# Kernel optimization log

Measured on AMD Instinct MI355X. Metric: run time of the kernel, lower is better.

Reference implementation:

```python
import jax, jax.numpy as jnp
import numpy as np

N_USERS = 500_000
N_ITEMS = 200_000
D_FEAT = 256
H = 32
N_EDGES = 2_000_000
NEG_SLOPE = 0.01


def _lin(k, out_dim, in_dim):
    return jax.random.normal(k, (out_dim, in_dim), jnp.float32) * (1.0 / np.sqrt(in_dim))


def setup_inputs() -> dict:
    key = jax.random.key(0)
    ks = jax.random.split(key, 24)
    src = jax.random.randint(ks[0], (N_EDGES,), 0, N_USERS)   # user ids
    dst = jax.random.randint(ks[1], (N_EDGES,), 0, N_ITEMS)   # product ids
    inp = {
        "user_ids": jnp.arange(N_USERS, dtype=jnp.int32),
        "product_ids": jnp.arange(N_ITEMS, dtype=jnp.int32),
        "product_features": jax.random.normal(ks[2], (N_ITEMS, D_FEAT), jnp.float32),
        "edge_rates": jnp.stack([src, dst]),      # user -> product
        "edge_rated_by": jnp.stack([dst, src]),   # product -> user (reverse)
        "user_emb": jax.random.normal(ks[3], (N_USERS, H), jnp.float32),
        "item_emb": jax.random.normal(ks[4], (N_ITEMS, H), jnp.float32),
        "feat_W": _lin(ks[5], H, D_FEAT),
        "feat_b": jnp.zeros((H,), jnp.float32),
    }
    # SAGEConv params: lin_l (neighbor, with bias), lin_r (root, no bias)
    names = ["up1", "pu1", "up2", "pu2"]  # up = user->product conv, pu = product->user conv
    for i, n in enumerate(names):
        inp[f"Wl_{n}"] = _lin(ks[6 + 3 * i], H, H)
        inp[f"bl_{n}"] = jnp.zeros((H,), jnp.float32)
        inp[f"Wr_{n}"] = _lin(ks[7 + 3 * i], H, H)
    return inp


def _sage(x_src, x_dst, edge_index, Wl, bl, Wr):
    # PyG SAGEConv, aggr='mean': lin_l(mean_j x_src[j]) + lin_r(x_dst)
    e_src, e_dst = edge_index[0], edge_index[1]
    n_dst = x_dst.shape[0]
    msg_sum = jax.ops.segment_sum(x_src[e_src], e_dst, num_segments=n_dst)
    cnt = jax.ops.segment_sum(jnp.ones_like(e_dst, dtype=x_src.dtype), e_dst, num_segments=n_dst)
    mean = msg_sum / jnp.maximum(cnt, 1.0)[:, None]
    return mean @ Wl.T + bl + x_dst @ Wr.T


def reference(user_ids, product_ids, product_features, edge_rates, edge_rated_by,
              user_emb, item_emb, feat_W, feat_b,
              Wl_up1, bl_up1, Wr_up1, Wl_pu1, bl_pu1, Wr_pu1,
              Wl_up2, bl_up2, Wr_up2, Wl_pu2, bl_pu2, Wr_pu2):
    lrelu = lambda x: jax.nn.leaky_relu(x, NEG_SLOPE)
    xu = user_emb[user_ids]                                    # [Nu, H]
    xp = item_emb[product_ids] + product_features @ feat_W.T + feat_b  # [Ni, H]

    # layer 1 (HeteroConv: each node type has exactly one incoming relation)
    p1 = lrelu(_sage(xu, xp, edge_rates, Wl_up1, bl_up1, Wr_up1))
    u1 = lrelu(_sage(xp, xu, edge_rated_by, Wl_pu1, bl_pu1, Wr_pu1))
    # layer 2
    p2 = lrelu(_sage(u1, p1, edge_rates, Wl_up2, bl_up2, Wr_up2))
    u2 = lrelu(_sage(p1, u1, edge_rated_by, Wl_pu2, bl_pu2, Wr_pu2))

    final_user = jnp.concatenate([xu, u1, u2], axis=1)   # [Nu, 3H]
    final_item = jnp.concatenate([xp, p1, p2], axis=1)   # [Ni, 3H]
    return final_user, final_item
```

## Files before the change

kernel.cpp:

```cpp
#include <hip/hip_runtime.h>

#define NU 500000
#define NI 200000
#define NN (NU + NI)
#define NE 2000000
#define HD 32
#define DF 256
#define OC 96

typedef float        f4 __attribute__((ext_vector_type(4)));
typedef unsigned int u2 __attribute__((ext_vector_type(2)));
typedef unsigned int u4v __attribute__((ext_vector_type(4)));
typedef unsigned short ushort_t;

__device__ __forceinline__ float lrelu(float v){ return v >= 0.f ? v : 0.01f*v; }

__device__ __forceinline__ unsigned int f2bf(float f){
  unsigned int u = __float_as_uint(f);
  u += 0x7fffu + ((u >> 16) & 1u);
  return u >> 16;
}
__device__ __forceinline__ float bflo(unsigned int u){ return __uint_as_float(u << 16); }
__device__ __forceinline__ float bfhi(unsigned int u){ return __uint_as_float(u & 0xffff0000u); }

__global__ void k_zero_i32(int* __restrict__ p, int n){
  int i = blockIdx.x*blockDim.x + threadIdx.x;
  if (i < n) p[i] = 0;
}

__global__ void k_init_user(const int* __restrict__ ids, const float* __restrict__ emb,
                            float* __restrict__ outu){
  int i = blockIdx.x*blockDim.x + threadIdx.x;
  if (i >= NU) return;
  int uid = ids[i];
  const f4* s = (const f4*)(emb + (size_t)uid*HD);
  f4* d = (f4*)(outu + (size_t)i*OC);
  #pragma unroll
  for (int q = 0; q < 8; ++q) {
    f4 v = __builtin_nontemporal_load(s + q);
    __builtin_nontemporal_store(v, d + q);
  }
}

__global__ __launch_bounds__(512) void k_init_item(
    const int* __restrict__ ids, const float* __restrict__ emb,
    const float* __restrict__ feat, const float* __restrict__ W,
    const float* __restrict__ bias, float* __restrict__ outi){
  __shared__ float combo[256*34];
  int t = threadIdx.x;
  int r = t & 255;
  int seg = __builtin_amdgcn_readfirstlane(t >> 8);
  int row = blockIdx.x*256 + r;
  bool valid = row < NI;
  float acc[HD];
  #pragma unroll
  for (int h = 0; h < HD; ++h) acc[h] = 0.f;

  if (valid) {
    const f4* f4p = (const f4*)(feat + (size_t)row*DF + seg*128);
    f4 a0 = __builtin_nontemporal_load(f4p);
    f4 a1 = __builtin_nontemporal_load(f4p + 1);
    for (int k0 = 0; k0 < 128; k0 += 8) {
      f4 n0 = {0,0,0,0}, n1 = {0,0,0,0};
      if (k0 + 8 < 128) {
        n0 = __builtin_nontemporal_load(f4p + (k0>>2) + 2);
        n1 = __builtin_nontemporal_load(f4p + (k0>>2) + 3);
      }
      float fv[8] = {a0.x,a0.y,a0.z,a0.w,a1.x,a1.y,a1.z,a1.w};
      #pragma unroll
      for (int kk = 0; kk < 8; ++kk) {
        #pragma unroll
        for (int h = 0; h < HD; ++h)
          acc[h] += fv[kk]*W[h*DF + seg*128 + k0 + kk];
      }
      a0 = n0; a1 = n1;
    }
  }
  if (seg == 1) {
    float2* c2 = (float2*)(combo + r*34);
    #pragma unroll
    for (int q = 0; q < 16; ++q) c2[q] = make_float2(acc[2*q], acc[2*q+1]);
  }
  __syncthreads();
  if (seg == 0 && valid) {
    const float2* c2 = (const float2*)(combo + r*34);
    #pragma unroll
    for (int q = 0; q < 16; ++q) { float2 v = c2[q]; acc[2*q] += v.x; acc[2*q+1] += v.y; }
    int pid = ids[row];
    const f4* ev = (const f4*)(emb + (size_t)pid*HD);
    const f4* bv = (const f4*)bias;
    f4* dst = (f4*)(outi + (size_t)row*OC);
    #pragma unroll
    for (int q = 0; q < 8; ++q) {
      f4 e = ev[q], b = bv[q];
      f4 o;
      o.x = acc[4*q+0]+e.x+b.x; o.y = acc[4*q+1]+e.y+b.y;
      o.z = acc[4*q+2]+e.z+b.z; o.w = acc[4*q+3]+e.w+b.w;
      __builtin_nontemporal_store(o, dst + q);
    }
  }
}

__global__ void k_deg(const int* __restrict__ esrc, const int* __restrict__ edst,
                      int* __restrict__ cnt){
  int e = blockIdx.x*blockDim.x + threadIdx.x;
  if (e >= NE) return;
  int u = __builtin_nontemporal_load(esrc + e);
  int p = __builtin_nontemporal_load(edst + e);
  atomicAdd(cnt + u, 1);
  atomicAdd(cnt + NU + p, 1);
}

__global__ void k_scan1(const int* __restrict__ cnt, int* __restrict__ off,
                        int* __restrict__ part, int n){
  __shared__ int s[256];
  int t = threadIdx.x, i = blockIdx.x*256 + t;
  int v = (i < n) ? cnt[i] : 0;
  s[t] = v; __syncthreads();
  for (int o = 1; o < 256; o <<= 1) {
    int x = (t >= o) ? s[t-o] : 0;
    __syncthreads(); s[t] += x; __syncthreads();
  }
  if (i < n) off[i] = s[t] - v;
  if (t == 255) part[blockIdx.x] = s[255];
}

__global__ void k_scan2(int* __restrict__ part, int nb){
  __shared__ int s[256];
  __shared__ int carry;
  int t = threadIdx.x;
  if (t == 0) carry = 0;
  __syncthreads();
  for (int c0 = 0; c0 < nb; c0 += 256) {
    int i = c0 + t;
    int v = (i < nb) ? part[i] : 0;
    s[t] = v; __syncthreads();
    for (int o = 1; o < 256; o <<= 1) {
      int x = (t >= o) ? s[t-o] : 0;
      __syncthreads(); s[t] += x; __syncthreads();
    }
    int total = s[255];
    if (i < nb) part[i] = carry + s[t] - v;
    __syncthreads();
    if (t == 0) carry += total;
    __syncthreads();
  }
}

__global__ void k_scan3(int* __restrict__ off, const int* __restrict__ part, int n){
  int i = blockIdx.x*256 + threadIdx.x;
  if (i < n) off[i] += part[blockIdx.x];
}

__global__ void k_scatter(const int* __restrict__ esrc, const int* __restrict__ edst,
                          const int* __restrict__ off, int* __restrict__ cur,
                          int* __restrict__ partner){
  int e = blockIdx.x*blockDim.x + threadIdx.x;
  if (e >= NE) return;
  int u = __builtin_nontemporal_load(esrc + e);
  int p = __builtin_nontemporal_load(edst + e);
  int s1 = off[u]      + atomicAdd(cur + u,      1);
  int s2 = off[NU + p] + atomicAdd(cur + NU + p, 1);
  partner[s1] = s2;
  partner[s2] = s1;
}

__global__ void k_mat(const float* __restrict__ srcbase, int scol, int n_src, int nodebase,
                      const int* __restrict__ off, const int* __restrict__ cnt,
                      const int* __restrict__ partner, ushort_t* __restrict__ edgeval,
                      int slotbase){
  int tid = blockIdx.x*256 + threadIdx.x;
  int node = tid >> 3;
  if (node >= n_src) return;
  int q = tid & 7;
  int gnode = nodebase + node;
  int deg = cnt[gnode];
  if (deg <= 0) return;
  int start = off[gnode];
  f4 v = __builtin_nontemporal_load((const f4*)(srcbase + (size_t)node*OC + scol) + q);
  u2 pv; pv.x = f2bf(v.x) | (f2bf(v.y) << 16); pv.y = f2bf(v.z) | (f2bf(v.w) << 16);
  u2* ev = (u2*)edgeval + q;
  int j = 0;
  for (; j + 4 <= deg; j += 4) {
    int s0 = __builtin_nontemporal_load(partner + start + j + 0) - slotbase;
    int s1 = __builtin_nontemporal_load(partner + start + j + 1) - slotbase;
    int s2 = __builtin_nontemporal_load(partner + start + j + 2) - slotbase;
    int s3 = __builtin_nontemporal_load(partner + start + j + 3) - slotbase;
    __builtin_nontemporal_store(pv, ev + (size_t)s0*8);
    __builtin_nontemporal_store(pv, ev + (size_t)s1*8);
    __builtin_nontemporal_store(pv, ev + (size_t)s2*8);
    __builtin_nontemporal_store(pv, ev + (size_t)s3*8);
  }
  for (; j < deg; ++j) {
    int s = __builtin_nontemporal_load(partner + start + j) - slotbase;
    __builtin_nontemporal_store(pv, ev + (size_t)s*8);
  }
}

__global__ void k_aggsum(const ushort_t* __restrict__ edgeval, int slotbase,
                         int n, int nodebase,
                         const int* __restrict__ off, const int* __restrict__ cnt,
                         ushort_t* __restrict__ meanb){
  int tid = blockIdx.x*256 + threadIdx.x;
  int node = tid >> 3;
  if (node >= n) return;
  int q = tid & 7;
  int gnode = nodebase + node;
  int deg = cnt[gnode];
  int start = off[gnode] - slotbase;
  const u2* ev = (const u2*)edgeval + q;
  f4 a0 = {0,0,0,0}, a1 = a0, a2 = a0, a3 = a0;
  int j = 0;
  for (; j + 4 <= deg; j += 4) {
    u2 r0 = ev[(size_t)(start+j+0)*8];
    u2 r1 = ev[(size_t)(start+j+1)*8];
    u2 r2 = ev[(size_t)(start+j+2)*8];
    u2 r3 = ev[(size_t)(start+j+3)*8];
    a0.x += bflo(r0.x); a0.y += bfhi(r0.x); a0.z += bflo(r0.y); a0.w += bfhi(r0.y);
    a1.x += bflo(r1.x); a1.y += bfhi(r1.x); a1.z += bflo(r1.y); a1.w += bfhi(r1.y);
    a2.x += bflo(r2.x); a2.y += bfhi(r2.x); a2.z += bflo(r2.y); a2.w += bfhi(r2.y);
    a3.x += bflo(r3.x); a3.y += bfhi(r3.x); a3.z += bflo(r3.y); a3.w += bfhi(r3.y);
  }
  for (; j < deg; ++j) {
    u2 r = ev[(size_t)(start+j)*8];
    a0.x += bflo(r.x); a0.y += bfhi(r.x); a0.z += bflo(r.y); a0.w += bfhi(r.y);
  }
  a0 += a1 + a2 + a3;
  float inv = (deg > 0) ? 1.f/(float)deg : 0.f;
  u2 pv;
  pv.x = f2bf(a0.x*inv) | (f2bf(a0.y*inv) << 16);
  pv.y = f2bf(a0.z*inv) | (f2bf(a0.w*inv) << 16);
  *((u2*)meanb + (size_t)node*8 + q) = pv;
}

__global__ void k_fin2(float* __restrict__ dstbase, int n,
                       const ushort_t* __restrict__ meanb, int xoff, int outoff,
                       const float* __restrict__ Wl, const float* __restrict__ bl,
                       const float* __restrict__ Wr){
  int i = blockIdx.x*blockDim.x + threadIdx.x;
  if (i >= n) return;
  float m[HD], x[HD];
  const u4v* mb = (const u4v*)(meanb + (size_t)i*HD);
  #pragma unroll
  for (int t = 0; t < 4; ++t) {
    u4v v = mb[t];
    m[8*t+0] = bflo(v.x); m[8*t+1] = bfhi(v.x);
    m[8*t+2] = bflo(v.y); m[8*t+3] = bfhi(v.y);
    m[8*t+4] = bflo(v.z); m[8*t+5] = bfhi(v.z);
    m[8*t+6] = bflo(v.w); m[8*t+7] = bfhi(v.w);
  }
  float* row = dstbase + (size_t)i*OC;
  #pragma unroll
  for (int qq = 0; qq < 8; ++qq) {
    f4 xx = *((const f4*)(row + xoff) + qq);
    x[4*qq+0]=xx.x; x[4*qq+1]=xx.y; x[4*qq+2]=xx.z; x[4*qq+3]=xx.w;
  }
  float y[HD];
  #pragma unroll
  for (int h = 0; h < HD; ++h) {
    float s = bl[h];
    #pragma unroll
    for (int j = 0; j < HD; ++j) s += m[j]*Wl[h*HD+j];
    #pragma unroll
    for (int j = 0; j < HD; ++j) s += x[j]*Wr[h*HD+j];
    y[h] = lrelu(s);
  }
  #pragma unroll
  for (int qq = 0; qq < 8; ++qq) {
    f4 yo; yo.x=y[4*qq+0]; yo.y=y[4*qq+1]; yo.z=y[4*qq+2]; yo.w=y[4*qq+3];
    __builtin_nontemporal_store(yo, (f4*)(row + outoff) + qq);
  }
}

__global__ void k_aggfin(float* __restrict__ dstbase, int n, int nodebase,
                         const ushort_t* __restrict__ edgeval, int slotbase,
                         int xoff, int outoff,
                         const int* __restrict__ off, const int* __restrict__ cnt,
                         const float* __restrict__ Wl, const float* __restrict__ bl,
                         const float* __restrict__ Wr){
  int tid = blockIdx.x*256 + threadIdx.x;
  int node = tid >> 3;
  if (node >= n) return;
  int q = tid & 7;
  int gnode = nodebase + node;
  int deg = cnt[gnode];
  int start = off[gnode] - slotbase;
  f4 xv = *((const f4*)(dstbase + (size_t)node*OC + xoff) + q);
  const u2* ev = (const u2*)edgeval + q;
  f4 a0 = {0,0,0,0};
  for (int j = 0; j < deg; ++j) {
    u2 r = ev[(size_t)(start+j)*8];
    a0.x += bflo(r.x); a0.y += bfhi(r.x); a0.z += bflo(r.y); a0.w += bfhi(r.y);
  }
  float inv = (deg > 0) ? 1.f/(float)deg : 0.f;
  float m0[4] = {a0.x*inv, a0.y*inv, a0.z*inv, a0.w*inv};
  float x0[4] = {xv.x, xv.y, xv.z, xv.w};
  bool b1 = (q & 1), b2 = (q & 2), b4 = (q & 4);
  float tm1[8], tx1[8];
  #pragma unroll
  for (int k = 0; k < 4; ++k) {
    float om = __shfl_xor(m0[k], 1), ox = __shfl_xor(x0[k], 1);
    tm1[k]   = b1 ? om    : m0[k];  tx1[k]   = b1 ? ox    : x0[k];
    tm1[k+4] = b1 ? m0[k] : om;     tx1[k+4] = b1 ? x0[k] : ox;
  }
  float tm2[16], tx2[16];
  #pragma unroll
  for (int k = 0; k < 8; ++k) {
    float om = __shfl_xor(tm1[k], 2), ox = __shfl_xor(tx1[k], 2);
    tm2[k]   = b2 ? om     : tm1[k];  tx2[k]   = b2 ? ox     : tx1[k];
    tm2[k+8] = b2 ? tm1[k] : om;      tx2[k+8] = b2 ? tx1[k] : ox;
  }
  float m[32], x[32];
  #pragma unroll
  for (int k = 0; k < 16; ++k) {
    float om = __shfl_xor(tm2[k], 4), ox = __shfl_xor(tx2[k], 4);
    m[k]    = b4 ? om     : tm2[k];  x[k]    = b4 ? ox     : tx2[k];
    m[k+16] = b4 ? tm2[k] : om;      x[k+16] = b4 ? tx2[k] : ox;
  }
  float y[4];
  #pragma unroll
  for (int k = 0; k < 4; ++k) {
    int h = q*4 + k;
    float s = bl[h];
    const f4* wl = (const f4*)(Wl + h*HD);
    const f4* wr = (const f4*)(Wr + h*HD);
    #pragma unroll
    for (int j4 = 0; j4 < 8; ++j4) {
      f4 wv = wl[j4];
      s += m[4*j4+0]*wv.x + m[4*j4+1]*wv.y + m[4*j4+2]*wv.z + m[4*j4+3]*wv.w;
    }
    #pragma unroll
    for (int j4 = 0; j4 < 8; ++j4) {
      f4 wv = wr[j4];
      s += x[4*j4+0]*wv.x + x[4*j4+1]*wv.y + x[4*j4+2]*wv.z + x[4*j4+3]*wv.w;
    }
    y[k] = lrelu(s);
  }
  f4 yo; yo.x = y[0]; yo.y = y[1]; yo.z = y[2]; yo.w = y[3];
  *((f4*)(dstbase + (size_t)node*OC + outoff) + q) = yo;
}

extern "C" void kernel_launch(void* const* d_in, const int* in_sizes, int n_in,
                              void* d_out, int out_size, void* d_ws, size_t ws_size,
                              hipStream_t stream) {
  const int*   user_ids = (const int*)d_in[0];
  const int*   prod_ids = (const int*)d_in[1];
  const float* feat     = (const float*)d_in[2];
  const int*   er       = (const int*)d_in[3];
  const float* uemb     = (const float*)d_in[5];
  const float* iemb     = (const float*)d_in[6];
  const float* fW       = (const float*)d_in[7];
  const float* fb       = (const float*)d_in[8];
  const float* Wl_up1 = (const float*)d_in[9];
  const float* bl_up1 = (const float*)d_in[10];
  const float* Wr_up1 = (const float*)d_in[11];
  const float* Wl_pu1 = (const float*)d_in[12];
  const float* bl_pu1 = (const float*)d_in[13];
  const float* Wr_pu1 = (const float*)d_in[14];
  const float* Wl_up2 = (const float*)d_in[15];
  const float* bl_up2 = (const float*)d_in[16];
  const float* Wr_up2 = (const float*)d_in[17];
  const float* Wl_pu2 = (const float*)d_in[18];
  const float* bl_pu2 = (const float*)d_in[19];
  const float* Wr_pu2 = (const float*)d_in[20];

  float* outu = (float*)d_out;
  float* outi = outu + (size_t)NU*OC;

  int* cnt  = (int*)d_ws;
  int* cur  = cnt + NN;
  int* off  = cur + NN;
  int* part = off + NN;
  int* pn   = part + 2736;
  size_t base_bytes = ((size_t)3*NN + 2736 + 2*(size_t)NE) * 4;
  size_t ev_off = (base_bytes + 255) & ~(size_t)255;
  ushort_t* edgeval = (ushort_t*)((char*)d_ws + ev_off);
  size_t mb_off = ev_off + (size_t)NE*64;
  ushort_t* meanb = (ushort_t*)((char*)d_ws + mb_off);
  bool have_mean = ws_size >= mb_off + (size_t)NU*64;

  const int* er_src = er;
  const int* er_dst = er + NE;

  const int B = 256;
  const int NB1 = (NN + 255)/256;
  const int GU8 = ((size_t)NU*8 + B - 1)/B, GI8 = ((size_t)NI*8 + B - 1)/B;
  const int GU1 = (NU + B - 1)/B,           GI1 = (NI + B - 1)/B;

  k_zero_i32<<<(2*NN + B - 1)/B, B, 0, stream>>>(cnt, 2*NN);
  k_deg<<<(NE + B - 1)/B, B, 0, stream>>>(er_src, er_dst, cnt);
  k_scan1<<<NB1, B, 0, stream>>>(cnt, off, part, NN);
  k_scan2<<<1, B, 0, stream>>>(part, NB1);
  k_scan3<<<NB1, B, 0, stream>>>(off, part, NN);
  k_scatter<<<(NE + B - 1)/B, B, 0, stream>>>(er_src, er_dst, off, cur, pn);

  k_init_user<<<GU1, B, 0, stream>>>(user_ids, uemb, outu);
  k_init_item<<<(NI + 255)/256, 512, 0, stream>>>(prod_ids, iemb, feat, fW, fb, outi);

  if (have_mean) {
    k_mat<<<GU8, B, 0, stream>>>(outu, 0, NU, 0, off, cnt, pn, edgeval, NE);
    k_aggsum<<<GI8, B, 0, stream>>>(edgeval, NE, NI, NU, off, cnt, meanb);
    k_fin2<<<GI1, B, 0, stream>>>(outi, NI, meanb, 0, 32, Wl_up1, bl_up1, Wr_up1);
    k_mat<<<GI8, B, 0, stream>>>(outi, 0, NI, NU, off, cnt, pn, edgeval, 0);
    k_aggsum<<<GU8, B, 0, stream>>>(edgeval, 0, NU, 0, off, cnt, meanb);
    k_fin2<<<GU1, B, 0, stream>>>(outu, NU, meanb, 0, 32, Wl_pu1, bl_pu1, Wr_pu1);
    k_mat<<<GU8, B, 0, stream>>>(outu, 32, NU, 0, off, cnt, pn, edgeval, NE);
    k_aggsum<<<GI8, B, 0, stream>>>(edgeval, NE, NI, NU, off, cnt, meanb);
    k_fin2<<<GI1, B, 0, stream>>>(outi, NI, meanb, 32, 64, Wl_up2, bl_up2, Wr_up2);
    k_mat<<<GI8, B, 0, stream>>>(outi, 32, NI, NU, off, cnt, pn, edgeval, 0);
    k_aggsum<<<GU8, B, 0, stream>>>(edgeval, 0, NU, 0, off, cnt, meanb);
    k_fin2<<<GU1, B, 0, stream>>>(outu, NU, meanb, 32, 64, Wl_pu2, bl_pu2, Wr_pu2);
  } else {
    k_mat<<<GU8, B, 0, stream>>>(outu, 0, NU, 0, off, cnt, pn, edgeval, NE);
    k_aggfin<<<GI8, B, 0, stream>>>(outi, NI, NU, edgeval, NE, 0, 32, off, cnt,
                                    Wl_up1, bl_up1, Wr_up1);
    k_mat<<<GI8, B, 0, stream>>>(outi, 0, NI, NU, off, cnt, pn, edgeval, 0);
    k_aggfin<<<GU8, B, 0, stream>>>(outu, NU, 0, edgeval, 0, 0, 32, off, cnt,
                                    Wl_pu1, bl_pu1, Wr_pu1);
    k_mat<<<GU8, B, 0, stream>>>(outu, 32, NU, 0, off, cnt, pn, edgeval, NE);
    k_aggfin<<<GI8, B, 0, stream>>>(outi, NI, NU, edgeval, NE, 32, 64, off, cnt,
                                    Wl_up2, bl_up2, Wr_up2);
    k_mat<<<GI8, B, 0, stream>>>(outi, 32, NI, NU, off, cnt, pn, edgeval, 0);
    k_aggfin<<<GU8, B, 0, stream>>>(outu, NU, 0, edgeval, 0, 32, 64, off, cnt,
                                    Wl_pu2, bl_pu2, Wr_pu2);
  }
}
```

Baseline: 1.764 ms.

## Fuse init with edge materialization, use MFMA for item features, merge aggregate+finalize

The user-embedding copy is fused with the first edge-value scatter, so the user table is written once and also packed into a compact bf16 table. The item feature projection now runs on bf16 MFMA tiles instead of scalar FMA. The separate aggregate, mean-buffer and finalize kernels are replaced by one kernel that stages per-node means in shared memory and also writes a bf16 copy of the layer-1 user output. The next scatter reads that compact table instead of the fp32 rows, and nontemporal hints are dropped. This cuts kernel launches and intermediate traffic, at the cost of bf16 rounding in the feature GEMM and a workspace size assumption that is no longer checked.

```diff
diff --git a/kernel.cpp b/kernel.cpp
--- a/kernel.cpp
+++ b/kernel.cpp
@@ -8,9 +8,9 @@
 #define DF 256
 #define OC 96
 
-typedef float        f4 __attribute__((ext_vector_type(4)));
-typedef unsigned int u2 __attribute__((ext_vector_type(2)));
-typedef unsigned int u4v __attribute__((ext_vector_type(4)));
+typedef float        f4  __attribute__((ext_vector_type(4)));
+typedef unsigned int u2  __attribute__((ext_vector_type(2)));
+typedef short        s8v __attribute__((ext_vector_type(8)));
 typedef unsigned short ushort_t;
 
 __device__ __forceinline__ float lrelu(float v){ return v >= 0.f ? v : 0.01f*v; }
@@ -23,82 +23,16 @@
 __device__ __forceinline__ float bflo(unsigned int u){ return __uint_as_float(u << 16); }
 __device__ __forceinline__ float bfhi(unsigned int u){ return __uint_as_float(u & 0xffff0000u); }
 
+__device__ __forceinline__ s8v pack8(f4 a, f4 b){
+  s8v r;
+  r[0]=(short)f2bf(a.x); r[1]=(short)f2bf(a.y); r[2]=(short)f2bf(a.z); r[3]=(short)f2bf(a.w);
+  r[4]=(short)f2bf(b.x); r[5]=(short)f2bf(b.y); r[6]=(short)f2bf(b.z); r[7]=(short)f2bf(b.w);
+  return r;
+}
+
 __global__ void k_zero_i32(int* __restrict__ p, int n){
   int i = blockIdx.x*blockDim.x + threadIdx.x;
   if (i < n) p[i] = 0;
-}
-
-__global__ void k_init_user(const int* __restrict__ ids, const float* __restrict__ emb,
-                            float* __restrict__ outu){
-  int i = blockIdx.x*blockDim.x + threadIdx.x;
-  if (i >= NU) return;
-  int uid = ids[i];
-  const f4* s = (const f4*)(emb + (size_t)uid*HD);
-  f4* d = (f4*)(outu + (size_t)i*OC);
-  #pragma unroll
-  for (int q = 0; q < 8; ++q) {
-    f4 v = __builtin_nontemporal_load(s + q);
-    __builtin_nontemporal_store(v, d + q);
-  }
-}
-
-__global__ __launch_bounds__(512) void k_init_item(
-    const int* __restrict__ ids, const float* __restrict__ emb,
-    const float* __restrict__ feat, const float* __restrict__ W,
-    const float* __restrict__ bias, float* __restrict__ outi){
-  __shared__ float combo[256*34];
-  int t = threadIdx.x;
-  int r = t & 255;
-  int seg = __builtin_amdgcn_readfirstlane(t >> 8);
-  int row = blockIdx.x*256 + r;
-  bool valid = row < NI;
-  float acc[HD];
-  #pragma unroll
-  for (int h = 0; h < HD; ++h) acc[h] = 0.f;
-
-  if (valid) {
-    const f4* f4p = (const f4*)(feat + (size_t)row*DF + seg*128);
-    f4 a0 = __builtin_nontemporal_load(f4p);
-    f4 a1 = __builtin_nontemporal_load(f4p + 1);
-    for (int k0 = 0; k0 < 128; k0 += 8) {
-      f4 n0 = {0,0,0,0}, n1 = {0,0,0,0};
-      if (k0 + 8 < 128) {
-        n0 = __builtin_nontemporal_load(f4p + (k0>>2) + 2);
-        n1 = __builtin_nontemporal_load(f4p + (k0>>2) + 3);
-      }
-      float fv[8] = {a0.x,a0.y,a0.z,a0.w,a1.x,a1.y,a1.z,a1.w};
-      #pragma unroll
-      for (int kk = 0; kk < 8; ++kk) {
-        #pragma unroll
-        for (int h = 0; h < HD; ++h)
-          acc[h] += fv[kk]*W[h*DF + seg*128 + k0 + kk];
-      }
-      a0 = n0; a1 = n1;
-    }
-  }
-  if (seg == 1) {
-    float2* c2 = (float2*)(combo + r*34);
-    #pragma unroll
-    for (int q = 0; q < 16; ++q) c2[q] = make_float2(acc[2*q], acc[2*q+1]);
-  }
-  __syncthreads();
-  if (seg == 0 && valid) {
-    const float2* c2 = (const float2*)(combo + r*34);
-    #pragma unroll
-    for (int q = 0; q < 16; ++q) { float2 v = c2[q]; acc[2*q] += v.x; acc[2*q+1] += v.y; }
-    int pid = ids[row];
-    const f4* ev = (const f4*)(emb + (size_t)pid*HD);
-    const f4* bv = (const f4*)bias;
-    f4* dst = (f4*)(outi + (size_t)row*OC);
-    #pragma unroll
-    for (int q = 0; q < 8; ++q) {
-      f4 e = ev[q], b = bv[q];
-      f4 o;
-      o.x = acc[4*q+0]+e.x+b.x; o.y = acc[4*q+1]+e.y+b.y;
-      o.z = acc[4*q+2]+e.z+b.z; o.w = acc[4*q+3]+e.w+b.w;
-      __builtin_nontemporal_store(o, dst + q);
-    }
-  }
 }
 
 __global__ void k_deg(const int* __restrict__ esrc, const int* __restrict__ edst,
@@ -165,10 +99,88 @@
   partner[s2] = s1;
 }
 
-__global__ void k_mat(const float* __restrict__ srcbase, int scol, int n_src, int nodebase,
-                      const int* __restrict__ off, const int* __restrict__ cnt,
-                      const int* __restrict__ partner, ushort_t* __restrict__ edgeval,
-                      int slotbase){
+__global__ void k_init_user_mat(const int* __restrict__ ids, const float* __restrict__ emb,
+                                float* __restrict__ outu, ushort_t* __restrict__ tbl,
+                                const int* __restrict__ off, const int* __restrict__ cnt,
+                                const int* __restrict__ partner,
+                                ushort_t* __restrict__ edgeval){
+  int tid = blockIdx.x*256 + threadIdx.x;
+  int node = tid >> 3;
+  if (node >= NU) return;
+  int q = tid & 7;
+  int uid = ids[node];
+  f4 v = *((const f4*)(emb + (size_t)uid*HD) + q);
+  *((f4*)(outu + (size_t)node*OC) + q) = v;
+  u2 pv; pv.x = f2bf(v.x) | (f2bf(v.y) << 16); pv.y = f2bf(v.z) | (f2bf(v.w) << 16);
+  ((u2*)tbl)[(size_t)node*8 + q] = pv;
+  int deg = cnt[node];
+  if (deg <= 0) return;
+  int start = off[node];
+  u2* ev = (u2*)edgeval + q;
+  int j = 0;
+  for (; j + 4 <= deg; j += 4) {
+    int s0 = __builtin_nontemporal_load(partner + start + j + 0) - NE;
+    int s1 = __builtin_nontemporal_load(partner + start + j + 1) - NE;
+    int s2 = __builtin_nontemporal_load(partner + start + j + 2) - NE;
+    int s3 = __builtin_nontemporal_load(partner + start + j + 3) - NE;
+    ev[(size_t)s0*8] = pv; ev[(size_t)s1*8] = pv;
+    ev[(size_t)s2*8] = pv; ev[(size_t)s3*8] = pv;
+  }
+  for (; j < deg; ++j) {
+    int s = __builtin_nontemporal_load(partner + start + j) - NE;
+    ev[(size_t)s*8] = pv;
+  }
+}
+
+__global__ __launch_bounds__(256) void k_init_item_mfma(
+    const int* __restrict__ ids, const float* __restrict__ emb,
+    const float* __restrict__ feat, const float* __restrict__ W,
+    const float* __restrict__ bias, float* __restrict__ outi){
+  int wave = threadIdx.x >> 6;
+  int lane = threadIdx.x & 63;
+  int tile = blockIdx.x*4 + wave;
+  int row0 = tile*16;
+  if (row0 >= NI) return;
+  int m = lane & 15, grp = lane >> 4;
+
+  s8v bfrag[16];
+  #pragma unroll
+  for (int ks = 0; ks < 8; ++ks) {
+    #pragma unroll
+    for (int nh = 0; nh < 2; ++nh) {
+      const float* wp = W + (size_t)(nh*16 + m)*DF + ks*32 + grp*8;
+      f4 w0 = *(const f4*)wp;
+      f4 w1 = *(const f4*)(wp + 4);
+      bfrag[ks*2 + nh] = pack8(w0, w1);
+    }
+  }
+
+  f4 acc0 = {0,0,0,0}, acc1 = {0,0,0,0};
+  const float* fr = feat + (size_t)(row0 + m)*DF + grp*8;
+  #pragma unroll
+  for (int ks = 0; ks < 8; ++ks) {
+    f4 a0 = *(const f4*)(fr + ks*32);
+    f4 a1 = *(const f4*)(fr + ks*32 + 4);
+    s8v af = pack8(a0, a1);
+    acc0 = __builtin_amdgcn_mfma_f32_16x16x32_bf16(af, bfrag[ks*2+0], acc0, 0, 0, 0);
+    acc1 = __builtin_amdgcn_mfma_f32_16x16x32_bf16(af, bfrag[ks*2+1], acc1, 0, 0, 0);
+  }
+
+  #pragma unroll
+  for (int j = 0; j < 4; ++j) {
+    int r = row0 + grp*4 + j;
+    int pid = ids[r];
+    float v0 = acc0[j] + emb[(size_t)pid*HD + m]      + bias[m];
+    float v1 = acc1[j] + emb[(size_t)pid*HD + 16 + m] + bias[16 + m];
+    outi[(size_t)r*OC + m]      = v0;
+    outi[(size_t)r*OC + 16 + m] = v1;
+  }
+}
+
+__global__ void k_mat_f32(const float* __restrict__ srcbase, int scol, int n_src, int nodebase,
+                          const int* __restrict__ off, const int* __restrict__ cnt,
+                          const int* __restrict__ partner, ushort_t* __restrict__ edgeval,
+                          int slotbase){
   int tid = blockIdx.x*256 + threadIdx.x;
   int node = tid >> 3;
   if (node >= n_src) return;
@@ -177,7 +189,7 @@
   int deg = cnt[gnode];
   if (deg <= 0) return;
   int start = off[gnode];
-  f4 v = __builtin_nontemporal_load((const f4*)(srcbase + (size_t)node*OC + scol) + q);
+  f4 v = *((const f4*)(srcbase + (size_t)node*OC + scol) + q);
   u2 pv; pv.x = f2bf(v.x) | (f2bf(v.y) << 16); pv.y = f2bf(v.z) | (f2bf(v.w) << 16);
   u2* ev = (u2*)edgeval + q;
   int j = 0;
@@ -186,137 +198,91 @@
     int s1 = __builtin_nontemporal_load(partner + start + j + 1) - slotbase;
     int s2 = __builtin_nontemporal_load(partner + start + j + 2) - slotbase;
     int s3 = __builtin_nontemporal_load(partner + start + j + 3) - slotbase;
-    __builtin_nontemporal_store(pv, ev + (size_t)s0*8);
-    __builtin_nontemporal_store(pv, ev + (size_t)s1*8);
-    __builtin_nontemporal_store(pv, ev + (size_t)s2*8);
-    __builtin_nontemporal_store(pv, ev + (size_t)s3*8);
+    ev[(size_t)s0*8] = pv; ev[(size_t)s1*8] = pv;
+    ev[(size_t)s2*8] = pv; ev[(size_t)s3*8] = pv;
   }
   for (; j < deg; ++j) {
     int s = __builtin_nontemporal_load(partner + start + j) - slotbase;
-    __builtin_nontemporal_store(pv, ev + (size_t)s*8);
-  }
-}
-
-__global__ void k_aggsum(const ushort_t* __restrict__ edgeval, int slotbase,
-                         int n, int nodebase,
-                         const int* __restrict__ off, const int* __restrict__ cnt,
-                         ushort_t* __restrict__ meanb){
+    ev[(size_t)s*8] = pv;
+  }
+}
+
+__global__ void k_mat_tbl(const ushort_t* __restrict__ tbl, int n_src, int nodebase,
+                          const int* __restrict__ off, const int* __restrict__ cnt,
+                          const int* __restrict__ partner, ushort_t* __restrict__ edgeval,
+                          int slotbase){
   int tid = blockIdx.x*256 + threadIdx.x;
   int node = tid >> 3;
-  if (node >= n) return;
+  if (node >= n_src) return;
   int q = tid & 7;
   int gnode = nodebase + node;
   int deg = cnt[gnode];
-  int start = off[gnode] - slotbase;
-  const u2* ev = (const u2*)edgeval + q;
-  f4 a0 = {0,0,0,0}, a1 = a0, a2 = a0, a3 = a0;
+  if (deg <= 0) return;
+  int start = off[gnode];
+  u2 pv = ((const u2*)tbl)[(size_t)node*8 + q];
+  u2* ev = (u2*)edgeval + q;
   int j = 0;
   for (; j + 4 <= deg; j += 4) {
-    u2 r0 = ev[(size_t)(start+j+0)*8];
-    u2 r1 = ev[(size_t)(start+j+1)*8];
-    u2 r2 = ev[(size_t)(start+j+2)*8];
-    u2 r3 = ev[(size_t)(start+j+3)*8];
-    a0.x += bflo(r0.x); a0.y += bfhi(r0.x); a0.z += bflo(r0.y); a0.w += bfhi(r0.y);
-    a1.x += bflo(r1.x); a1.y += bfhi(r1.x); a1.z += bflo(r1.y); a1.w += bfhi(r1.y);
-    a2.x += bflo(r2.x); a2.y += bfhi(r2.x); a2.z += bflo(r2.y); a2.w += bfhi(r2.y);
-    a3.x += bflo(r3.x); a3.y += bfhi(r3.x); a3.z += bflo(r3.y); a3.w += bfhi(r3.y);
+    int s0 = __builtin_nontemporal_load(partner + start + j + 0) - slotbase;
+    int s1 = __builtin_nontemporal_load(partner + start + j + 1) - slotbase;
+    int s2 = __builtin_nontemporal_load(partner + start + j + 2) - slotbase;
+    int s3 = __builtin_nontemporal_load(partner + start + j + 3) - slotbase;
+    ev[(size_t)s0*8] = pv; ev[(size_t)s1*8] = pv;
+    ev[(size_t)s2*8] = pv; ev[(size_t)s3*8] = pv;
   }
   for (; j < deg; ++j) {
-    u2 r = ev[(size_t)(start+j)*8];
-    a0.x += bflo(r.x); a0.y += bfhi(r.x); a0.z += bflo(r.y); a0.w += bfhi(r.y);
-  }
-  a0 += a1 + a2 + a3;
+    int s = __builtin_nontemporal_load(partner + start + j) - slotbase;
+    ev[(size_t)s*8] = pv;
+  }
+}
+
+__global__ __launch_bounds__(256) void k_aggfin2(
+    float* __restrict__ dstbase, int n, int nodebase,
+    const ushort_t* __restrict__ edgeval, int slotbase,
+    int xoff, int outoff,
+    const int* __restrict__ off, const int* __restrict__ cnt,
+    const float* __restrict__ Wl, const float* __restrict__ bl,
+    const float* __restrict__ Wr, ushort_t* __restrict__ tblout){
+  __shared__ float mbuf[32*36];
+  __shared__ float xbuf[32*36];
+  int t = threadIdx.x;
+  int nl = t >> 3;
+  int q = t & 7;
+  int node = blockIdx.x*32 + nl;
+  bool valid = node < n;
+  f4 a0 = {0,0,0,0}, a1 = a0, a2 = a0, a3 = a0, xv = a0;
+  int deg = 0;
+  if (valid) {
+    int g = nodebase + node;
+    deg = cnt[g];
+    int start = off[g] - slotbase;
+    xv = *((const f4*)(dstbase + (size_t)node*OC + xoff) + q);
+    const u2* ev = (const u2*)edgeval + q;
+    int j = 0;
+    for (; j + 4 <= deg; j += 4) {
+      u2 r0 = ev[(size_t)(start+j+0)*8];
+      u2 r1 = ev[(size_t)(start+j+1)*8];
+      u2 r2 = ev[(size_t)(start+j+2)*8];
+      u2 r3 = ev[(size_t)(start+j+3)*8];
+      a0.x += bflo(r0.x); a0.y += bfhi(r0.x); a0.z += bflo(r0.y); a0.w += bfhi(r0.y);
+      a1.x += bflo(r1.x); a1.y += bfhi(r1.x); a1.z += bflo(r1.y); a1.w += bfhi(r1.y);
+      a2.x += bflo(r2.x); a2.y += bfhi(r2.x); a2.z += bflo(r2.y); a2.w += bfhi(r2.y);
+      a3.x += bflo(r3.x); a3.y += bfhi(r3.x); a3.z += bflo(r3.y); a3.w += bfhi(r3.y);
+    }
+    for (; j < deg; ++j) {
+      u2 r = ev[(size_t)(start+j)*8];
+      a0.x += bflo(r.x); a0.y += bfhi(r.x); a0.z += bflo(r.y); a0.w += bfhi(r.y);
+    }
+    a0 += a1 + a2 + a3;
+  }
   float inv = (deg > 0) ? 1.f/(float)deg : 0.f;
-  u2 pv;
-  pv.x = f2bf(a0.x*inv) | (f2bf(a0.y*inv) << 16);
-  pv.y = f2bf(a0.z*inv) | (f2bf(a0.w*inv) << 16);
-  *((u2*)meanb + (size_t)node*8 + q) = pv;
-}
-
-__global__ void k_fin2(float* __restrict__ dstbase, int n,
-                       const ushort_t* __restrict__ meanb, int xoff, int outoff,
-                       const float* __restrict__ Wl, const float* __restrict__ bl,
-                       const float* __restrict__ Wr){
-  int i = blockIdx.x*blockDim.x + threadIdx.x;
-  if (i >= n) return;
-  float m[HD], x[HD];
-  const u4v* mb = (const u4v*)(meanb + (size_t)i*HD);
-  #pragma unroll
-  for (int t = 0; t < 4; ++t) {
-    u4v v = mb[t];
-    m[8*t+0] = bflo(v.x); m[8*t+1] = bfhi(v.x);
-    m[8*t+2] = bflo(v.y); m[8*t+3] = bfhi(v.y);
-    m[8*t+4] = bflo(v.z); m[8*t+5] = bfhi(v.z);
-    m[8*t+6] = bflo(v.w); m[8*t+7] = bfhi(v.w);
-  }
-  float* row = dstbase + (size_t)i*OC;
-  #pragma unroll
-  for (int qq = 0; qq < 8; ++qq) {
-    f4 xx = *((const f4*)(row + xoff) + qq);
-    x[4*qq+0]=xx.x; x[4*qq+1]=xx.y; x[4*qq+2]=xx.z; x[4*qq+3]=xx.w;
-  }
-  float y[HD];
-  #pragma unroll
-  for (int h = 0; h < HD; ++h) {
-    float s = bl[h];
-    #pragma unroll
-    for (int j = 0; j < HD; ++j) s += m[j]*Wl[h*HD+j];
-    #pragma unroll
-    for (int j = 0; j < HD; ++j) s += x[j]*Wr[h*HD+j];
-    y[h] = lrelu(s);
-  }
-  #pragma unroll
-  for (int qq = 0; qq < 8; ++qq) {
-    f4 yo; yo.x=y[4*qq+0]; yo.y=y[4*qq+1]; yo.z=y[4*qq+2]; yo.w=y[4*qq+3];
-    __builtin_nontemporal_store(yo, (f4*)(row + outoff) + qq);
-  }
-}
-
-__global__ void k_aggfin(float* __restrict__ dstbase, int n, int nodebase,
-                         const ushort_t* __restrict__ edgeval, int slotbase,
-                         int xoff, int outoff,
-                         const int* __restrict__ off, const int* __restrict__ cnt,
-                         const float* __restrict__ Wl, const float* __restrict__ bl,
-                         const float* __restrict__ Wr){
-  int tid = blockIdx.x*256 + threadIdx.x;
-  int node = tid >> 3;
-  if (node >= n) return;
-  int q = tid & 7;
-  int gnode = nodebase + node;
-  int deg = cnt[gnode];
-  int start = off[gnode] - slotbase;
-  f4 xv = *((const f4*)(dstbase + (size_t)node*OC + xoff) + q);
-  const u2* ev = (const u2*)edgeval + q;
-  f4 a0 = {0,0,0,0};
-  for (int j = 0; j < deg; ++j) {
-    u2 r = ev[(size_t)(start+j)*8];
-    a0.x += bflo(r.x); a0.y += bfhi(r.x); a0.z += bflo(r.y); a0.w += bfhi(r.y);
-  }
-  float inv = (deg > 0) ? 1.f/(float)deg : 0.f;
-  float m0[4] = {a0.x*inv, a0.y*inv, a0.z*inv, a0.w*inv};
-  float x0[4] = {xv.x, xv.y, xv.z, xv.w};
-  bool b1 = (q & 1), b2 = (q & 2), b4 = (q & 4);
-  float tm1[8], tx1[8];
-  #pragma unroll
-  for (int k = 0; k < 4; ++k) {
-    float om = __shfl_xor(m0[k], 1), ox = __shfl_xor(x0[k], 1);
-    tm1[k]   = b1 ? om    : m0[k];  tx1[k]   = b1 ? ox    : x0[k];
-    tm1[k+4] = b1 ? m0[k] : om;     tx1[k+4] = b1 ? x0[k] : ox;
-  }
-  float tm2[16], tx2[16];
-  #pragma unroll
-  for (int k = 0; k < 8; ++k) {
-    float om = __shfl_xor(tm1[k], 2), ox = __shfl_xor(tx1[k], 2);
-    tm2[k]   = b2 ? om     : tm1[k];  tx2[k]   = b2 ? ox     : tx1[k];
-    tm2[k+8] = b2 ? tm1[k] : om;      tx2[k+8] = b2 ? tx1[k] : ox;
-  }
-  float m[32], x[32];
-  #pragma unroll
-  for (int k = 0; k < 16; ++k) {
-    float om = __shfl_xor(tm2[k], 4), ox = __shfl_xor(tx2[k], 4);
-    m[k]    = b4 ? om     : tm2[k];  x[k]    = b4 ? ox     : tx2[k];
-    m[k+16] = b4 ? tm2[k] : om;      x[k+16] = b4 ? tx2[k] : ox;
-  }
+  f4 mv; mv.x = a0.x*inv; mv.y = a0.y*inv; mv.z = a0.z*inv; mv.w = a0.w*inv;
+  *(f4*)(mbuf + nl*36 + q*4) = mv;
+  *(f4*)(xbuf + nl*36 + q*4) = xv;
+  __syncthreads();
+  if (!valid) return;
+  const f4* mr = (const f4*)(mbuf + nl*36);
+  const f4* xr = (const f4*)(xbuf + nl*36);
   float y[4];
   #pragma unroll
   for (int k = 0; k < 4; ++k) {
@@ -326,18 +292,24 @@
     const f4* wr = (const f4*)(Wr + h*HD);
     #pragma unroll
     for (int j4 = 0; j4 < 8; ++j4) {
-      f4 wv = wl[j4];
-      s += m[4*j4+0]*wv.x + m[4*j4+1]*wv.y + m[4*j4+2]*wv.z + m[4*j4+3]*wv.w;
+      f4 mm = mr[j4], wv = wl[j4];
+      s += mm.x*wv.x + mm.y*wv.y + mm.z*wv.z + mm.w*wv.w;
     }
     #pragma unroll
     for (int j4 = 0; j4 < 8; ++j4) {
-      f4 wv = wr[j4];
-      s += x[4*j4+0]*wv.x + x[4*j4+1]*wv.y + x[4*j4+2]*wv.z + x[4*j4+3]*wv.w;
+      f4 xx = xr[j4], wv = wr[j4];
+      s += xx.x*wv.x + xx.y*wv.y + xx.z*wv.z + xx.w*wv.w;
     }
     y[k] = lrelu(s);
   }
   f4 yo; yo.x = y[0]; yo.y = y[1]; yo.z = y[2]; yo.w = y[3];
   *((f4*)(dstbase + (size_t)node*OC + outoff) + q) = yo;
+  if (tblout) {
+    u2 pv;
+    pv.x = f2bf(y[0]) | (f2bf(y[1]) << 16);
+    pv.y = f2bf(y[2]) | (f2bf(y[3]) << 16);
+    ((u2*)tblout)[(size_t)node*8 + q] = pv;
+  }
 }
 
 extern "C" void kernel_launch(void* const* d_in, const int* in_sizes, int n_in,
@@ -375,9 +347,7 @@
   size_t base_bytes = ((size_t)3*NN + 2736 + 2*(size_t)NE) * 4;
   size_t ev_off = (base_bytes + 255) & ~(size_t)255;
   ushort_t* edgeval = (ushort_t*)((char*)d_ws + ev_off);
-  size_t mb_off = ev_off + (size_t)NE*64;
-  ushort_t* meanb = (ushort_t*)((char*)d_ws + mb_off);
-  bool have_mean = ws_size >= mb_off + (size_t)NU*64;
+  ushort_t* tblA    = (ushort_t*)((char*)d_ws + ev_off + (size_t)NE*64);
 
   const int* er_src = er;
   const int* er_dst = er + NE;
@@ -385,7 +355,7 @@
   const int B = 256;
   const int NB1 = (NN + 255)/256;
   const int GU8 = ((size_t)NU*8 + B - 1)/B, GI8 = ((size_t)NI*8 + B - 1)/B;
-  const int GU1 = (NU + B - 1)/B,           GI1 = (NI + B - 1)/B;
+  const int GU32 = (NU + 31)/32, GI32 = (NI + 31)/32;
 
   k_zero_i32<<<(2*NN + B - 1)/B, B, 0, stream>>>(cnt, 2*NN);
   k_deg<<<(NE + B - 1)/B, B, 0, stream>>>(er_src, er_dst, cnt);
@@ -394,34 +364,18 @@
   k_scan3<<<NB1, B, 0, stream>>>(off, part, NN);
   k_scatter<<<(NE + B - 1)/B, B, 0, stream>>>(er_src, er_dst, off, cur, pn);
 
-  k_init_user<<<GU1, B, 0, stream>>>(user_ids, uemb, outu);
-  k_init_item<<<(NI + 255)/256, 512, 0, stream>>>(prod_ids, iemb, feat, fW, fb, outi);
-
-  if (have_mean) {
-    k_mat<<<GU8, B, 0, stream>>>(outu, 0, NU, 0, off, cnt, pn, edgeval, NE);
-    k_aggsum<<<GI8, B, 0, stream>>>(edgeval, NE, NI, NU, off, cnt, meanb);
-    k_fin2<<<GI1, B, 0, stream>>>(outi, NI, meanb, 0, 32, Wl_up1, bl_up1, Wr_up1);
-    k_mat<<<GI8, B, 0, stream>>>(outi, 0, NI, NU, off, cnt, pn, edgeval, 0);
-    k_aggsum<<<GU8, B, 0, stream>>>(edgeval, 0, NU, 0, off, cnt, meanb);
-    k_fin2<<<GU1, B, 0, stream>>>(outu, NU, meanb, 0, 32, Wl_pu1, bl_pu1, Wr_pu1);
-    k_mat<<<GU8, B, 0, stream>>>(outu, 32, NU, 0, off, cnt, pn, edgeval, NE);
-    k_aggsum<<<GI8, B, 0, stream>>>(edgeval, NE, NI, NU, off, cnt, meanb);
-    k_fin2<<<GI1, B, 0, stream>>>(outi, NI, meanb, 32, 64, Wl_up2, bl_up2, Wr_up2);
-    k_mat<<<GI8, B, 0, stream>>>(outi, 32, NI, NU, off, cnt, pn, edgeval, 0);
-    k_aggsum<<<GU8, B, 0, stream>>>(edgeval, 0, NU, 0, off, cnt, meanb);
-    k_fin2<<<GU1, B, 0, stream>>>(outu, NU, meanb, 32, 64, Wl_pu2, bl_pu2, Wr_pu2);
-  } else {
-    k_mat<<<GU8, B, 0, stream>>>(outu, 0, NU, 0, off, cnt, pn, edgeval, NE);
-    k_aggfin<<<GI8, B, 0, stream>>>(outi, NI, NU, edgeval, NE, 0, 32, off, cnt,
-                                    Wl_up1, bl_up1, Wr_up1);
-    k_mat<<<GI8, B, 0, stream>>>(outi, 0, NI, NU, off, cnt, pn, edgeval, 0);
-    k_aggfin<<<GU8, B, 0, stream>>>(outu, NU, 0, edgeval, 0, 0, 32, off, cnt,
-                                    Wl_pu1, bl_pu1, Wr_pu1);
-    k_mat<<<GU8, B, 0, stream>>>(outu, 32, NU, 0, off, cnt, pn, edgeval, NE);
-    k_aggfin<<<GI8, B, 0, stream>>>(outi, NI, NU, edgeval, NE, 32, 64, off, cnt,
-                                    Wl_up2, bl_up2, Wr_up2);
-    k_mat<<<GI8, B, 0, stream>>>(outi, 32, NI, NU, off, cnt, pn, edgeval, 0);
-    k_aggfin<<<GU8, B, 0, stream>>>(outu, NU, 0, edgeval, 0, 32, 64, off, cnt,
-                                    Wl_pu2, bl_pu2, Wr_pu2);
-  }
-}
+  k_init_user_mat<<<GU8, B, 0, stream>>>(user_ids, uemb, outu, tblA, off, cnt, pn, edgeval);
+  k_init_item_mfma<<<(NI + 63)/64, 256, 0, stream>>>(prod_ids, iemb, feat, fW, fb, outi);
+
+  k_aggfin2<<<GI32, B, 0, stream>>>(outi, NI, NU, edgeval, NE, 0, 32, off, cnt,
+                                    Wl_up1, bl_up1, Wr_up1, (ushort_t*)nullptr);
+  k_mat_f32<<<GI8, B, 0, stream>>>(outi, 0, NI, NU, off, cnt, pn, edgeval, 0);
+  k_aggfin2<<<GU32, B, 0, stream>>>(outu, NU, 0, edgeval, 0, 0, 32, off, cnt,
+                                    Wl_pu1, bl_pu1, Wr_pu1, tblA);
+  k_mat_tbl<<<GU8, B, 0, stream>>>(tblA, NU, 0, off, cnt, pn, edgeval, NE);
+  k_aggfin2<<<GI32, B, 0, stream>>>(outi, NI, NU, edgeval, NE, 32, 64, off, cnt,
+                                    Wl_up2, bl_up2, Wr_up2, (ushort_t*)nullptr);
+  k_mat_f32<<<GI8, B, 0, stream>>>(outi, 32, NI, NU, off, cnt, pn, edgeval, 0);
+  k_aggfin2<<<GU32, B, 0, stream>>>(outu, NU, 0, edgeval, 0, 32, 64, off, cnt,
+                                    Wl_pu2, bl_pu2, Wr_pu2, (ushort_t*)nullptr);
+}
```

Result: slower. 2.035 ms (+15.3%).
